# Optimization experiments

Hardware: AMD Instinct MI355X
Metric: run time of the kernel (lower is better)

## Reference

```python
import jax, jax.numpy as jnp
import numpy as np

T, D, E, K, F = 512, 2048, 64, 8, 768  # tokens, hidden, experts, top_k, moe_intermediate

def setup_inputs() -> dict:
    key = jax.random.key(0)
    k0, k1, k2, k3, k4 = jax.random.split(key, 5)
    std = 0.02
    return {
        "hidden_states": jax.random.normal(k0, (T, D), dtype=jnp.float32),
        "gate_w": jax.random.normal(k1, (D, E), dtype=jnp.float32) * std,
        "w_gate": jax.random.normal(k2, (E, D, F), dtype=jnp.float32) * std,  # per-expert gate proj
        "w_up":   jax.random.normal(k3, (E, D, F), dtype=jnp.float32) * std,  # per-expert up proj
        "w_down": jax.random.normal(k4, (E, F, D), dtype=jnp.float32) * std,  # per-expert down proj
    }

def reference(hidden_states, gate_w, w_gate, w_up, w_down):
    x = hidden_states  # [T, D]
    # Router: gate linear -> softmax -> top-k -> renormalize (norm_topk_prob=True)
    router_logits = x @ gate_w                      # [T, E]
    probs = jax.nn.softmax(router_logits, axis=-1)  # [T, E]
    topk_w, topk_idx = jax.lax.top_k(probs, K)      # [T, K]
    topk_w = topk_w / jnp.sum(topk_w, axis=-1, keepdims=True)
    # Combine weights as dense [T, E] scatter (zero for unrouted experts)
    cw = jnp.zeros((T, E), dtype=x.dtype).at[jnp.arange(T)[:, None], topk_idx].set(topk_w)
    # Experts: SwiGLU MLP per expert, dense dispatch then weighted combine
    g = jnp.einsum('td,edf->etf', x, w_gate)        # [E, T, F]
    u = jnp.einsum('td,edf->etf', x, w_up)          # [E, T, F]
    h = jax.nn.silu(g) * u                          # [E, T, F]
    y = jnp.einsum('etf,efd->etd', h, w_down)       # [E, T, D]
    out = jnp.einsum('te,etd->td', cw, y)           # [T, D]
    return out
```

## Files before the change

kernel.cpp:

```cpp
#include <hip/hip_runtime.h>
#include <hip/hip_bf16.h>

#define T_TOK 512
#define D_DIM 2048
#define E_NUM 64
#define K_TOP 8
#define F_DIM 768

typedef __bf16 bf16x8 __attribute__((ext_vector_type(8)));
typedef float  f32x4  __attribute__((ext_vector_type(4)));

#define AS1 __attribute__((address_space(1)))
#define AS3 __attribute__((address_space(3)))

__device__ __forceinline__ void gll16(const void* g, void* l) {
    __builtin_amdgcn_global_load_lds((const AS1 uint32_t*)g, (AS3 uint32_t*)l, 16, 0, 0);
}

#define VM_WAIT_I(N) asm volatile("s_waitcnt vmcnt(" #N ")" ::: "memory")
#define VM_WAIT(N) VM_WAIT_I(N)

#define PIPE_STEP(WN, BUF, DOSTG, KN)            \
    do {                                          \
        VM_WAIT(WN);                              \
        __builtin_amdgcn_sched_barrier(0);        \
        __builtin_amdgcn_s_barrier();             \
        consume(BUF);                             \
        __builtin_amdgcn_s_barrier();             \
        __builtin_amdgcn_sched_barrier(0);        \
        if (DOSTG) stage(BUF, KN);                \
    } while (0)

#define WS_IDS   4096
#define WS_PW    139264
#define WS_XBF   155648
#define WS_H     2252800
#define WS_Y     8544256

__global__ void zero_cnt_kernel(int* __restrict__ cnt) {
    if (threadIdx.x < E_NUM) cnt[threadIdx.x] = 0;
}

__global__ __launch_bounds__(256) void xcvt_kernel(
        const float* __restrict__ x, __bf16* __restrict__ xb) {
    const size_t i = ((size_t)blockIdx.x * 256 + threadIdx.x) * 8;
    const float4 a = *(const float4*)(x + i);
    const float4 b = *(const float4*)(x + i + 4);
    bf16x8 v;
    v[0]=(__bf16)a.x; v[1]=(__bf16)a.y; v[2]=(__bf16)a.z; v[3]=(__bf16)a.w;
    v[4]=(__bf16)b.x; v[5]=(__bf16)b.y; v[6]=(__bf16)b.z; v[7]=(__bf16)b.w;
    *(uint4*)(xb + i) = __builtin_bit_cast(uint4, v);
}

__global__ __launch_bounds__(256) void router_kernel(
        const float* __restrict__ x, const float* __restrict__ gw,
        float* __restrict__ pair_w, int* __restrict__ cnt, int* __restrict__ ids) {
    const int t   = blockIdx.x;
    const int tid = threadIdx.x;
    const int c   = tid >> 4;
    const int g   = tid & 15;

    const float* xr  = x + (size_t)t * D_DIM + c * 128;
    const float4* gr = (const float4*)(gw + (size_t)(c * 128) * E_NUM + g * 4);

    f32x4 acc; acc[0]=0.f; acc[1]=0.f; acc[2]=0.f; acc[3]=0.f;
    #pragma unroll 8
    for (int k = 0; k < 128; k++) {
        const float xv = xr[k];
        const float4 wv = gr[(size_t)k * 16];
        acc[0] += xv * wv.x; acc[1] += xv * wv.y;
        acc[2] += xv * wv.z; acc[3] += xv * wv.w;
    }
    __shared__ f32x4 part[16][16];
    part[c][g] = acc;
    __syncthreads();
    if (tid < 64) {
        const int e = tid;
        float logit = 0.f;
        #pragma unroll
        for (int cc = 0; cc < 16; cc++) logit += part[cc][e >> 2][e & 3];
        float cur = logit;
        float selV[8]; int selE[8];
        #pragma unroll
        for (int i = 0; i < 8; i++) {
            float bv = cur; int bi = e;
            #pragma unroll
            for (int off = 32; off > 0; off >>= 1) {
                float ov = __shfl_xor(bv, off);
                int   oi = __shfl_xor(bi, off);
                if (ov > bv || (ov == bv && oi < bi)) { bv = ov; bi = oi; }
            }
            selV[i] = bv; selE[i] = bi;
            if (e == bi) cur = -INFINITY;
        }
        const float m = selV[0];
        float sum = 0.f;
        #pragma unroll
        for (int i = 0; i < 8; i++) sum += __expf(selV[i] - m);
        float myW = 0.f; int myE = 0;
        #pragma unroll
        for (int i = 0; i < 8; i++) {
            if (e == i) { myW = __expf(selV[i] - m) / sum; myE = selE[i]; }
        }
        if (e < 8) {
            pair_w[t * K_TOP + e] = myW;
            int pos = atomicAdd(&cnt[myE], 1);
            ids[myE * T_TOK + pos] = t * K_TOP + e;
        }
    }
}

template<int KDIM, int ASTR, int BSTR, int MODE>
__global__ __launch_bounds__(256, 3) void gemm_kernel(
        const __bf16* __restrict__ Abase, const float* __restrict__ Bw,
        const int* __restrict__ cnt, const int* __restrict__ ids,
        const __bf16* __restrict__ Gin, __bf16* __restrict__ Out) {
    constexpr int NCT = BSTR / 64;
    constexpr int NWG = NCT * E_NUM;
    constexpr int CHK = NWG / 8;
    const int bid = blockIdx.y * NCT + blockIdx.x;
    const int wg  = (bid & 7) * CHK + (bid >> 3);
    const int e   = wg / NCT;
    const int ct  = wg % NCT;
    const int n = cnt[e];
    if (n <= 0) return;

    const int tid  = threadIdx.x;
    const int lane = tid & 63;
    const int w    = tid >> 6;
    const int g16  = lane >> 4;
    const int l16  = lane & 15;

    __shared__ __align__(16) char lds[3][16384];

    const float* bsrc = Bw + (size_t)e * KDIM * BSTR
                      + (size_t)(tid >> 4) * BSTR + ct * 64 + (tid & 15) * 4;
    const int ach = tid >> 7;
    const int arw = tid & 127;
    const int col = ct * 64 + w * 16 + l16;

    for (int mt = 0; mt * 128 < n; mt++) {
        const int ap  = mt * 128 + arw;
        const int aid = ids[(size_t)e * T_TOK + (ap < n ? ap : n - 1)];
        const __bf16* asrc = Abase + (size_t)(MODE < 2 ? (aid >> 3) : aid) * ASTR;

        f32x4 acc[8];
        #pragma unroll
        for (int m = 0; m < 8; m++) { acc[m][0]=0.f; acc[m][1]=0.f; acc[m][2]=0.f; acc[m][3]=0.f; }

        auto stage = [&](int buf, int ks) {
            char* L = lds[buf];
            gll16(asrc + ks * 32 + ach * 8,        L + ach * 2048 + arw * 16);
            gll16(asrc + ks * 32 + (ach + 2) * 8,  L + (ach + 2) * 2048 + arw * 16);
            gll16(bsrc + (size_t)(ks * 32) * BSTR,      L + 8192 + tid * 16);
            gll16(bsrc + (size_t)(ks * 32 + 16) * BSTR, L + 8192 + 4096 + tid * 16);
        };
        auto consume = [&](int buf) {
            const char* L = lds[buf];
            const float* Bf = (const float*)(L + 8192);
            bf16x8 bf;
            #pragma unroll
            for (int i = 0; i < 8; i++)
                bf[i] = (__bf16)Bf[(g16 * 8 + i) * 64 + w * 16 + l16];
            #pragma unroll
            for (int m = 0; m < 8; m++) {
                bf16x8 af = __builtin_bit_cast(bf16x8,
                    *(const uint4*)(L + g16 * 2048 + (m * 16 + l16) * 16));
                acc[m] = __builtin_amdgcn_mfma_f32_16x16x32_bf16(af, bf, acc[m], 0, 0, 0);
            }
        };

        stage(0, 0); stage(1, 1); stage(2, 2);

        constexpr int NK = KDIM / 32;
        for (int ks = 0; ks < NK - 3; ks++) {
            PIPE_STEP(8, ks % 3, true, ks + 3);
        }
        PIPE_STEP(8, (NK - 3) % 3, false, 0);
        PIPE_STEP(4, (NK - 2) % 3, false, 0);
        PIPE_STEP(0, (NK - 1) % 3, false, 0);

        #pragma unroll
        for (int m = 0; m < 8; m++) {
            #pragma unroll
            for (int r = 0; r < 4; r++) {
                const int p = mt * 128 + m * 16 + g16 * 4 + r;
                if (p < n) {
                    const int rid = ids[(size_t)e * T_TOK + p];
                    float v = acc[m][r];
                    if (MODE == 1) {
                        const float g = (float)Gin[(size_t)rid * BSTR + col];
                        v *= g / (1.f + __expf(-g));
                    }
                    Out[(size_t)rid * BSTR + col] = (__bf16)v;
                }
            }
        }
    }
}

__global__ __launch_bounds__(256) void combine_kernel(
        const __bf16* __restrict__ Y, const float* __restrict__ pw,
        float* __restrict__ out) {
    const int t   = blockIdx.x;
    const int tid = threadIdx.x;
    const int d0  = tid * 8;
    float acc[8];
    #pragma unroll
    for (int j = 0; j < 8; j++) acc[j] = 0.f;
    #pragma unroll
    for (int k = 0; k < K_TOP; k++) {
        const float wgt = pw[t * K_TOP + k];
        bf16x8 v = *(const bf16x8*)(Y + (size_t)(t * K_TOP + k) * D_DIM + d0);
        #pragma unroll
        for (int j = 0; j < 8; j++) acc[j] += wgt * (float)v[j];
    }
    #pragma unroll
    for (int j = 0; j < 8; j++) out[(size_t)t * D_DIM + d0 + j] = acc[j];
}

extern "C" void kernel_launch(void* const* d_in, const int* in_sizes, int n_in,
                              void* d_out, int out_size, void* d_ws, size_t ws_size,
                              hipStream_t stream) {
    const float* x      = (const float*)d_in[0];
    const float* gw     = (const float*)d_in[1];
    const float* w_gate = (const float*)d_in[2];
    const float* w_up   = (const float*)d_in[3];
    const float* w_down = (const float*)d_in[4];
    float* out = (float*)d_out;

    char* ws = (char*)d_ws;
    int*    cnt = (int*)(ws);
    int*    ids = (int*)(ws + WS_IDS);
    float*  pw  = (float*)(ws + WS_PW);
    __bf16* xbf = (__bf16*)(ws + WS_XBF);
    __bf16* H   = (__bf16*)(ws + WS_H);
    __bf16* Y   = (__bf16*)(ws + WS_Y);
    __bf16* G   = (__bf16*)(ws + WS_Y);

    zero_cnt_kernel<<<1, 64, 0, stream>>>(cnt);
    xcvt_kernel<<<T_TOK * D_DIM / (256 * 8), 256, 0, stream>>>(x, xbf);
    router_kernel<<<T_TOK, 256, 0, stream>>>(x, gw, pw, cnt, ids);
    gemm_kernel<D_DIM, D_DIM, F_DIM, 0><<<dim3(F_DIM / 64, E_NUM), 256, 0, stream>>>(
        xbf, w_gate, cnt, ids, nullptr, G);
    gemm_kernel<D_DIM, D_DIM, F_DIM, 1><<<dim3(F_DIM / 64, E_NUM), 256, 0, stream>>>(
        xbf, w_up, cnt, ids, G, H);
    gemm_kernel<F_DIM, F_DIM, D_DIM, 2><<<dim3(D_DIM / 64, E_NUM), 256, 0, stream>>>(
        H, w_down, cnt, ids, nullptr, Y);
    combine_kernel<<<T_TOK, 256, 0, stream>>>(Y, pw, out);
}
```

Before: 363.5 us.

## Pre-gather routed activations into contiguous per-expert bf16 tiles for GEMMs

Replaces the global x-to-bf16 conversion with gather kernels that write each expert's routed tokens (and later H rows) into contiguous, k-step-blocked bf16 tiles. The GEMM A-loads then become fully coalesced 1 KB chunks instead of per-row scattered gathers through the ids table. The consume step also preloads all A fragments before the MFMAs and raises wave priority around them. This costs two extra gather passes and much larger workspace traffic (per-expert tiles of up to 128-row blocks).

```diff
diff --git a/kernel.cpp b/kernel.cpp
--- a/kernel.cpp
+++ b/kernel.cpp
@@ -33,23 +33,19 @@
 
 #define WS_IDS   4096
 #define WS_PW    139264
-#define WS_XBF   155648
-#define WS_H     2252800
-#define WS_Y     8544256
+#define WS_H     262144
+#define WS_G     7340032
+#define WS_Y     14680064
+#define WS_AXT   33554432
+#define WS_AHT   176160768
+
+#define AXT_TILE  524288
+#define AXT_ESTR  2097152
+#define AHT_TILE  196608
+#define AHT_ESTR  786432
 
 __global__ void zero_cnt_kernel(int* __restrict__ cnt) {
     if (threadIdx.x < E_NUM) cnt[threadIdx.x] = 0;
-}
-
-__global__ __launch_bounds__(256) void xcvt_kernel(
-        const float* __restrict__ x, __bf16* __restrict__ xb) {
-    const size_t i = ((size_t)blockIdx.x * 256 + threadIdx.x) * 8;
-    const float4 a = *(const float4*)(x + i);
-    const float4 b = *(const float4*)(x + i + 4);
-    bf16x8 v;
-    v[0]=(__bf16)a.x; v[1]=(__bf16)a.y; v[2]=(__bf16)a.z; v[3]=(__bf16)a.w;
-    v[4]=(__bf16)b.x; v[5]=(__bf16)b.y; v[6]=(__bf16)b.z; v[7]=(__bf16)b.w;
-    *(uint4*)(xb + i) = __builtin_bit_cast(uint4, v);
 }
 
 __global__ __launch_bounds__(256) void router_kernel(
@@ -110,9 +106,76 @@
     }
 }
 
-template<int KDIM, int ASTR, int BSTR, int MODE>
+__global__ __launch_bounds__(256) void atile_x_kernel(
+        const float* __restrict__ x, const int* __restrict__ cnt,
+        const int* __restrict__ ids, __bf16* __restrict__ axt) {
+    const int e  = blockIdx.z;
+    const int mt = blockIdx.y;
+    const int n  = cnt[e];
+    if (n <= 0 || mt * 128 >= n) return;
+    const int ks0 = blockIdx.x * 8;
+    const int tid = threadIdx.x;
+    const int row = tid >> 1;
+    const int cp  = (tid & 1) * 2;
+
+    int j = mt * 128 + row;
+    if (j >= n) j = n - 1;
+    const int tok = ids[(size_t)e * T_TOK + j] >> 3;
+    const float* src = x + (size_t)tok * D_DIM + cp * 8;
+    char* dst = (char*)axt + (size_t)e * AXT_ESTR + (size_t)mt * AXT_TILE
+              + row * 64 + cp * 16;
+
+    #pragma unroll
+    for (int ksl = 0; ksl < 8; ksl++) {
+        const int ks = ks0 + ksl;
+        const float4 a = *(const float4*)(src + ks * 32);
+        const float4 b = *(const float4*)(src + ks * 32 + 4);
+        const float4 c = *(const float4*)(src + ks * 32 + 8);
+        const float4 d = *(const float4*)(src + ks * 32 + 12);
+        bf16x8 v0, v1;
+        v0[0]=(__bf16)a.x; v0[1]=(__bf16)a.y; v0[2]=(__bf16)a.z; v0[3]=(__bf16)a.w;
+        v0[4]=(__bf16)b.x; v0[5]=(__bf16)b.y; v0[6]=(__bf16)b.z; v0[7]=(__bf16)b.w;
+        v1[0]=(__bf16)c.x; v1[1]=(__bf16)c.y; v1[2]=(__bf16)c.z; v1[3]=(__bf16)c.w;
+        v1[4]=(__bf16)d.x; v1[5]=(__bf16)d.y; v1[6]=(__bf16)d.z; v1[7]=(__bf16)d.w;
+        uint4* o = (uint4*)(dst + (size_t)ks * 8192);
+        o[0] = __builtin_bit_cast(uint4, v0);
+        o[1] = __builtin_bit_cast(uint4, v1);
+    }
+}
+
+__global__ __launch_bounds__(256) void atile_h_kernel(
+        const __bf16* __restrict__ H, const int* __restrict__ cnt,
+        const int* __restrict__ ids, __bf16* __restrict__ aht) {
+    const int e  = blockIdx.z;
+    const int mt = blockIdx.y;
+    const int n  = cnt[e];
+    if (n <= 0 || mt * 128 >= n) return;
+    const int ks0 = blockIdx.x * 8;
+    const int tid = threadIdx.x;
+    const int row = tid >> 1;
+    const int cp  = (tid & 1) * 2;
+
+    int j = mt * 128 + row;
+    if (j >= n) j = n - 1;
+    const int rid = ids[(size_t)e * T_TOK + j];
+    const char* src = (const char*)(H + (size_t)rid * F_DIM) + cp * 16;
+    char* dst = (char*)aht + (size_t)e * AHT_ESTR + (size_t)mt * AHT_TILE
+              + row * 64 + cp * 16;
+
+    #pragma unroll
+    for (int ksl = 0; ksl < 8; ksl++) {
+        const int ks = ks0 + ksl;
+        const uint4 v0 = *(const uint4*)(src + ks * 64);
+        const uint4 v1 = *(const uint4*)(src + ks * 64 + 16);
+        uint4* o = (uint4*)(dst + (size_t)ks * 8192);
+        o[0] = v0;
+        o[1] = v1;
+    }
+}
+
+template<int NK, int BSTR, int ATILE, int AESTR, int MODE>
 __global__ __launch_bounds__(256, 3) void gemm_kernel(
-        const __bf16* __restrict__ Abase, const float* __restrict__ Bw,
+        const char* __restrict__ Atl, const float* __restrict__ Bw,
         const int* __restrict__ cnt, const int* __restrict__ ids,
         const __bf16* __restrict__ Gin, __bf16* __restrict__ Out) {
     constexpr int NCT = BSTR / 64;
@@ -133,16 +196,14 @@
 
     __shared__ __align__(16) char lds[3][16384];
 
-    const float* bsrc = Bw + (size_t)e * KDIM * BSTR
+    const float* bsrc = Bw + (size_t)e * NK * 32 * BSTR
                       + (size_t)(tid >> 4) * BSTR + ct * 64 + (tid & 15) * 4;
-    const int ach = tid >> 7;
-    const int arw = tid & 127;
+    const char* atl_e = Atl + (size_t)e * AESTR;
     const int col = ct * 64 + w * 16 + l16;
+    const int aoff = (w * 2 + (tid & 64 ? 1 : 0)) * 0;
 
     for (int mt = 0; mt * 128 < n; mt++) {
-        const int ap  = mt * 128 + arw;
-        const int aid = ids[(size_t)e * T_TOK + (ap < n ? ap : n - 1)];
-        const __bf16* asrc = Abase + (size_t)(MODE < 2 ? (aid >> 3) : aid) * ASTR;
+        const char* atile = atl_e + (size_t)mt * ATILE;
 
         f32x4 acc[8];
         #pragma unroll
@@ -150,8 +211,9 @@
 
         auto stage = [&](int buf, int ks) {
             char* L = lds[buf];
-            gll16(asrc + ks * 32 + ach * 8,        L + ach * 2048 + arw * 16);
-            gll16(asrc + ks * 32 + (ach + 2) * 8,  L + (ach + 2) * 2048 + arw * 16);
+            const char* as = atile + (size_t)ks * 8192;
+            gll16(as + (w + 0) * 1024 + lane * 16, L + (w + 0) * 1024 + lane * 16);
+            gll16(as + (w + 4) * 1024 + lane * 16, L + (w + 4) * 1024 + lane * 16);
             gll16(bsrc + (size_t)(ks * 32) * BSTR,      L + 8192 + tid * 16);
             gll16(bsrc + (size_t)(ks * 32 + 16) * BSTR, L + 8192 + 4096 + tid * 16);
         };
@@ -162,17 +224,20 @@
             #pragma unroll
             for (int i = 0; i < 8; i++)
                 bf[i] = (__bf16)Bf[(g16 * 8 + i) * 64 + w * 16 + l16];
-            #pragma unroll
-            for (int m = 0; m < 8; m++) {
-                bf16x8 af = __builtin_bit_cast(bf16x8,
-                    *(const uint4*)(L + g16 * 2048 + (m * 16 + l16) * 16));
-                acc[m] = __builtin_amdgcn_mfma_f32_16x16x32_bf16(af, bf, acc[m], 0, 0, 0);
-            }
+            bf16x8 af[8];
+            #pragma unroll
+            for (int m = 0; m < 8; m++)
+                af[m] = __builtin_bit_cast(bf16x8,
+                    *(const uint4*)(L + (m * 16 + l16) * 64 + g16 * 16));
+            __builtin_amdgcn_s_setprio(1);
+            #pragma unroll
+            for (int m = 0; m < 8; m++)
+                acc[m] = __builtin_amdgcn_mfma_f32_16x16x32_bf16(af[m], bf, acc[m], 0, 0, 0);
+            __builtin_amdgcn_s_setprio(0);
         };
 
         stage(0, 0); stage(1, 1); stage(2, 2);
 
-        constexpr int NK = KDIM / 32;
         for (int ks = 0; ks < NK - 3; ks++) {
             PIPE_STEP(8, ks % 3, true, ks + 3);
         }
@@ -233,19 +298,24 @@
     int*    cnt = (int*)(ws);
     int*    ids = (int*)(ws + WS_IDS);
     float*  pw  = (float*)(ws + WS_PW);
-    __bf16* xbf = (__bf16*)(ws + WS_XBF);
     __bf16* H   = (__bf16*)(ws + WS_H);
+    __bf16* G   = (__bf16*)(ws + WS_G);
     __bf16* Y   = (__bf16*)(ws + WS_Y);
-    __bf16* G   = (__bf16*)(ws + WS_Y);
+    __bf16* axt = (__bf16*)(ws + WS_AXT);
+    __bf16* aht = (__bf16*)(ws + WS_AHT);
 
     zero_cnt_kernel<<<1, 64, 0, stream>>>(cnt);
-    xcvt_kernel<<<T_TOK * D_DIM / (256 * 8), 256, 0, stream>>>(x, xbf);
     router_kernel<<<T_TOK, 256, 0, stream>>>(x, gw, pw, cnt, ids);
-    gemm_kernel<D_DIM, D_DIM, F_DIM, 0><<<dim3(F_DIM / 64, E_NUM), 256, 0, stream>>>(
-        xbf, w_gate, cnt, ids, nullptr, G);
-    gemm_kernel<D_DIM, D_DIM, F_DIM, 1><<<dim3(F_DIM / 64, E_NUM), 256, 0, stream>>>(
-        xbf, w_up, cnt, ids, G, H);
-    gemm_kernel<F_DIM, F_DIM, D_DIM, 2><<<dim3(D_DIM / 64, E_NUM), 256, 0, stream>>>(
-        H, w_down, cnt, ids, nullptr, Y);
+    atile_x_kernel<<<dim3(8, 4, E_NUM), 256, 0, stream>>>(x, cnt, ids, axt);
+    gemm_kernel<64, F_DIM, AXT_TILE, AXT_ESTR, 0>
+        <<<dim3(F_DIM / 64, E_NUM), 256, 0, stream>>>(
+        (const char*)axt, w_gate, cnt, ids, nullptr, G);
+    gemm_kernel<64, F_DIM, AXT_TILE, AXT_ESTR, 1>
+        <<<dim3(F_DIM / 64, E_NUM), 256, 0, stream>>>(
+        (const char*)axt, w_up, cnt, ids, G, H);
+    atile_h_kernel<<<dim3(3, 4, E_NUM), 256, 0, stream>>>(H, cnt, ids, aht);
+    gemm_kernel<24, D_DIM, AHT_TILE, AHT_ESTR, 2>
+        <<<dim3(D_DIM / 64, E_NUM), 256, 0, stream>>>(
+        (const char*)aht, w_down, cnt, ids, nullptr, Y);
     combine_kernel<<<T_TOK, 256, 0, stream>>>(Y, pw, out);
 }
```

Measured after the change: 374.5 us. +3.0%, slower.

## Fuse gate and up projections into one dual-B GEMM; widen down-proj tiles

Applied to the files above, without the earlier changes.

Merges the gate and up expert GEMMs into a single kernel that loads both weight tiles per K-step and shares the A tile. The SwiGLU is applied in the epilogue, which removes one launch, one pass over A, and the G intermediate round-trip through memory. The down projection now computes 128 output columns per workgroup, reusing each A fragment for two MFMAs. The pipeline drops from triple to double buffering at 24KB per stage and adds s_setprio around the MFMA loop. The trade-off is twice the accumulator registers and less latency hiding from the shallower pipeline.

```diff
diff --git a/kernel.cpp b/kernel.cpp
--- a/kernel.cpp
+++ b/kernel.cpp
@@ -110,12 +110,12 @@
     }
 }
 
-template<int KDIM, int ASTR, int BSTR, int MODE>
-__global__ __launch_bounds__(256, 3) void gemm_kernel(
-        const __bf16* __restrict__ Abase, const float* __restrict__ Bw,
-        const int* __restrict__ cnt, const int* __restrict__ ids,
-        const __bf16* __restrict__ Gin, __bf16* __restrict__ Out) {
-    constexpr int NCT = BSTR / 64;
+template<int NK, int BSTR, int MODE>
+__global__ __launch_bounds__(256, 3) void gemm2_kernel(
+        const __bf16* __restrict__ Abase, const float* __restrict__ B0w,
+        const float* __restrict__ B1w, const int* __restrict__ cnt,
+        const int* __restrict__ ids, __bf16* __restrict__ Out) {
+    constexpr int NCT = (MODE == 0) ? (BSTR / 64) : (BSTR / 128);
     constexpr int NWG = NCT * E_NUM;
     constexpr int CHK = NWG / 8;
     const int bid = blockIdx.y * NCT + blockIdx.x;
@@ -131,54 +131,68 @@
     const int g16  = lane >> 4;
     const int l16  = lane & 15;
 
-    __shared__ __align__(16) char lds[3][16384];
-
-    const float* bsrc = Bw + (size_t)e * KDIM * BSTR
-                      + (size_t)(tid >> 4) * BSTR + ct * 64 + (tid & 15) * 4;
+    __shared__ __align__(16) char lds[2][24576];
+
+    const int bcol0 = (MODE == 0) ? ct * 64 : ct * 128;
+    const int bcol1 = (MODE == 0) ? ct * 64 : ct * 128 + 64;
+    const float* b0 = B0w + (size_t)e * NK * 32 * BSTR
+                    + (size_t)(tid >> 4) * BSTR + bcol0 + (tid & 15) * 4;
+    const float* b1 = B1w + (size_t)e * NK * 32 * BSTR
+                    + (size_t)(tid >> 4) * BSTR + bcol1 + (tid & 15) * 4;
     const int ach = tid >> 7;
     const int arw = tid & 127;
-    const int col = ct * 64 + w * 16 + l16;
+    const int ci  = w * 16 + l16;
 
     for (int mt = 0; mt * 128 < n; mt++) {
         const int ap  = mt * 128 + arw;
         const int aid = ids[(size_t)e * T_TOK + (ap < n ? ap : n - 1)];
-        const __bf16* asrc = Abase + (size_t)(MODE < 2 ? (aid >> 3) : aid) * ASTR;
-
-        f32x4 acc[8];
-        #pragma unroll
-        for (int m = 0; m < 8; m++) { acc[m][0]=0.f; acc[m][1]=0.f; acc[m][2]=0.f; acc[m][3]=0.f; }
+        const __bf16* asrc = Abase + (size_t)(MODE == 0 ? (aid >> 3) : aid)
+                                   * (MODE == 0 ? D_DIM : F_DIM);
+
+        f32x4 acc0[8], acc1[8];
+        #pragma unroll
+        for (int m = 0; m < 8; m++) {
+            acc0[m][0]=0.f; acc0[m][1]=0.f; acc0[m][2]=0.f; acc0[m][3]=0.f;
+            acc1[m][0]=0.f; acc1[m][1]=0.f; acc1[m][2]=0.f; acc1[m][3]=0.f;
+        }
 
         auto stage = [&](int buf, int ks) {
             char* L = lds[buf];
             gll16(asrc + ks * 32 + ach * 8,        L + ach * 2048 + arw * 16);
             gll16(asrc + ks * 32 + (ach + 2) * 8,  L + (ach + 2) * 2048 + arw * 16);
-            gll16(bsrc + (size_t)(ks * 32) * BSTR,      L + 8192 + tid * 16);
-            gll16(bsrc + (size_t)(ks * 32 + 16) * BSTR, L + 8192 + 4096 + tid * 16);
+            gll16(b0 + (size_t)(ks * 32) * BSTR,      L + 8192 + tid * 16);
+            gll16(b0 + (size_t)(ks * 32 + 16) * BSTR, L + 8192 + 4096 + tid * 16);
+            gll16(b1 + (size_t)(ks * 32) * BSTR,      L + 16384 + tid * 16);
+            gll16(b1 + (size_t)(ks * 32 + 16) * BSTR, L + 16384 + 4096 + tid * 16);
         };
         auto consume = [&](int buf) {
             const char* L = lds[buf];
-            const float* Bf = (const float*)(L + 8192);
-            bf16x8 bf;
-            #pragma unroll
-            for (int i = 0; i < 8; i++)
-                bf[i] = (__bf16)Bf[(g16 * 8 + i) * 64 + w * 16 + l16];
+            const float* B0f = (const float*)(L + 8192);
+            const float* B1f = (const float*)(L + 16384);
+            bf16x8 bf0, bf1;
+            #pragma unroll
+            for (int i = 0; i < 8; i++) {
+                bf0[i] = (__bf16)B0f[(g16 * 8 + i) * 64 + ci];
+                bf1[i] = (__bf16)B1f[(g16 * 8 + i) * 64 + ci];
+            }
+            __builtin_amdgcn_s_setprio(1);
             #pragma unroll
             for (int m = 0; m < 8; m++) {
                 bf16x8 af = __builtin_bit_cast(bf16x8,
                     *(const uint4*)(L + g16 * 2048 + (m * 16 + l16) * 16));
-                acc[m] = __builtin_amdgcn_mfma_f32_16x16x32_bf16(af, bf, acc[m], 0, 0, 0);
-            }
+                acc0[m] = __builtin_amdgcn_mfma_f32_16x16x32_bf16(af, bf0, acc0[m], 0, 0, 0);
+                acc1[m] = __builtin_amdgcn_mfma_f32_16x16x32_bf16(af, bf1, acc1[m], 0, 0, 0);
+            }
+            __builtin_amdgcn_s_setprio(0);
         };
 
-        stage(0, 0); stage(1, 1); stage(2, 2);
-
-        constexpr int NK = KDIM / 32;
-        for (int ks = 0; ks < NK - 3; ks++) {
-            PIPE_STEP(8, ks % 3, true, ks + 3);
-        }
-        PIPE_STEP(8, (NK - 3) % 3, false, 0);
-        PIPE_STEP(4, (NK - 2) % 3, false, 0);
-        PIPE_STEP(0, (NK - 1) % 3, false, 0);
+        stage(0, 0); stage(1, 1);
+
+        for (int ks = 0; ks < NK - 2; ks++) {
+            PIPE_STEP(6, ks & 1, true, ks + 2);
+        }
+        PIPE_STEP(6, NK & 1, false, 0);
+        PIPE_STEP(0, (NK - 1) & 1, false, 0);
 
         #pragma unroll
         for (int m = 0; m < 8; m++) {
@@ -187,12 +201,14 @@
                 const int p = mt * 128 + m * 16 + g16 * 4 + r;
                 if (p < n) {
                     const int rid = ids[(size_t)e * T_TOK + p];
-                    float v = acc[m][r];
-                    if (MODE == 1) {
-                        const float g = (float)Gin[(size_t)rid * BSTR + col];
-                        v *= g / (1.f + __expf(-g));
+                    if (MODE == 0) {
+                        const float g = acc0[m][r], u = acc1[m][r];
+                        const float hv = (g / (1.f + __expf(-g))) * u;
+                        Out[(size_t)rid * F_DIM + ct * 64 + ci] = (__bf16)hv;
+                    } else {
+                        Out[(size_t)rid * D_DIM + ct * 128 + ci]      = (__bf16)acc0[m][r];
+                        Out[(size_t)rid * D_DIM + ct * 128 + 64 + ci] = (__bf16)acc1[m][r];
                     }
-                    Out[(size_t)rid * BSTR + col] = (__bf16)v;
                 }
             }
         }
@@ -236,16 +252,13 @@
     __bf16* xbf = (__bf16*)(ws + WS_XBF);
     __bf16* H   = (__bf16*)(ws + WS_H);
     __bf16* Y   = (__bf16*)(ws + WS_Y);
-    __bf16* G   = (__bf16*)(ws + WS_Y);
 
     zero_cnt_kernel<<<1, 64, 0, stream>>>(cnt);
     xcvt_kernel<<<T_TOK * D_DIM / (256 * 8), 256, 0, stream>>>(x, xbf);
     router_kernel<<<T_TOK, 256, 0, stream>>>(x, gw, pw, cnt, ids);
-    gemm_kernel<D_DIM, D_DIM, F_DIM, 0><<<dim3(F_DIM / 64, E_NUM), 256, 0, stream>>>(
-        xbf, w_gate, cnt, ids, nullptr, G);
-    gemm_kernel<D_DIM, D_DIM, F_DIM, 1><<<dim3(F_DIM / 64, E_NUM), 256, 0, stream>>>(
-        xbf, w_up, cnt, ids, G, H);
-    gemm_kernel<F_DIM, F_DIM, D_DIM, 2><<<dim3(D_DIM / 64, E_NUM), 256, 0, stream>>>(
-        H, w_down, cnt, ids, nullptr, Y);
+    gemm2_kernel<64, F_DIM, 0><<<dim3(F_DIM / 64, E_NUM), 256, 0, stream>>>(
+        xbf, w_gate, w_up, cnt, ids, H);
+    gemm2_kernel<24, D_DIM, 1><<<dim3(D_DIM / 128, E_NUM), 256, 0, stream>>>(
+        H, w_down, w_down, cnt, ids, Y);
     combine_kernel<<<T_TOK, 256, 0, stream>>>(Y, pw, out);
 }
```

Result: faster. 303.8 us (-16.4%).
